# Performance work log

Measured on AMD Instinct MI355X. Metric: run time of the kernel, lower is better.

## Reference

```python
import jax, jax.numpy as jnp
import numpy as np

BIAS = 1.0
SIGMA = 0.5
EPS = 1e-5


def mrf_loss(gen, target):
    # gen, target: [B, C, H, W]
    mean_t = jnp.mean(target, axis=1, keepdims=True)
    gf = gen - mean_t
    tf = target - mean_t
    gn = gf / jnp.linalg.norm(gf, axis=1, keepdims=True)
    tn = tf / jnp.linalg.norm(tf, axis=1, keepdims=True)
    B, C, H, W = target.shape
    # 1x1 patches of target, ordered by spatial position (matches unfold h,w order)
    patches = tn.transpose(0, 2, 3, 1).reshape(B, H * W, C)  # [B, P, C]
    # per-sample conv2d with 1x1 kernels == batched GEMM
    sim = jnp.einsum('bpc,bchw->bphw', patches, gn)  # [B, P, H, W]
    cosine_dist = -(sim - 1.0) / 2.0
    relative = cosine_dist / (jnp.min(cosine_dist, axis=1, keepdims=True) + EPS)
    dist = jnp.exp((BIAS - relative) / SIGMA)
    cs = dist / jnp.sum(dist, axis=1, keepdims=True)
    k_max = jnp.max(cs.reshape(B, H * W, -1), axis=2)  # [B, P]
    div_mrf = jnp.mean(k_max, axis=1)  # [B]
    return jnp.sum(-jnp.log(div_mrf))


def setup_inputs() -> dict:
    key = jax.random.key(0)
    k1, k2, k3, k4 = jax.random.split(key, 4)
    return {
        'gen_relu3_2': jax.random.normal(k1, (4, 256, 64, 64), dtype=jnp.float32),
        'tar_relu3_2': jax.random.normal(k2, (4, 256, 64, 64), dtype=jnp.float32),
        'gen_relu4_2': jax.random.normal(k3, (4, 512, 32, 32), dtype=jnp.float32),
        'tar_relu4_2': jax.random.normal(k4, (4, 512, 32, 32), dtype=jnp.float32),
    }


def reference(gen_relu3_2, tar_relu3_2, gen_relu4_2, tar_relu4_2):
    # style layers: relu3_2 (w=1.0), relu4_2 (w=1.0); content layers: relu4_2 (w=1.0)
    m3 = mrf_loss(gen_relu3_2, tar_relu3_2)
    m4 = mrf_loss(gen_relu4_2, tar_relu4_2)
    style_loss = (1.0 * m3 + 1.0 * m4) * 1.0  # l_s = 1.0
    content_loss = (1.0 * m4) * 1.0           # l_c = 1.0
    return style_loss + content_loss
```

## Files before the change

kernel.cpp:

```cpp
#include <hip/hip_runtime.h>
#include <math.h>


#define MRF_EPS 1e-5f
#define LOG2E 1.44269504088896340736f

typedef __attribute__((ext_vector_type(8))) short bf16x8;
typedef __attribute__((ext_vector_type(4))) float f32x4;
typedef unsigned short ushort_t;
struct __align__(8) ushort4_t { ushort_t x, y, z, w; };
struct __align__(16) ushort8_t { ushort_t v[8]; };

__device__ __forceinline__ ushort_t f2bf(float x) {
    unsigned u = __float_as_uint(x);
    u += 0x7FFFu + ((u >> 16) & 1u);
    return (ushort_t)(u >> 16);
}
__device__ __forceinline__ float bf2f(ushort_t u) {
    return __uint_as_float(((unsigned)u) << 16);
}

typedef __attribute__((address_space(1))) const unsigned int gu32;
typedef __attribute__((address_space(3))) unsigned int lu32;
__device__ __forceinline__ void gload16(const ushort_t* g, ushort_t* l) {
    __builtin_amdgcn_global_load_lds((gu32*)(uintptr_t)g, (lu32*)(uintptr_t)l,
                                     16, 0, 0);
}

template <int C>
__device__ __forceinline__ void prep_body(
    const float* __restrict__ gen, const float* __restrict__ tar,
    ushort_t* __restrict__ gnT, ushort_t* __restrict__ tnT,
    int S, int b, int bx, char* __restrict__ smem) {
    constexpr int KN = C / 64;
    constexpr int KC = C / 8;
    constexpr int CP = C + 8;
    const int tid = threadIdx.x, pq = tid & 3, cs = tid >> 2;
    const int s0 = bx * 16;

    f32x4* red  = (f32x4*)smem;
    f32x4* red2 = (f32x4*)(smem + 16384);
    ushort_t* tileG = (ushort_t*)smem;
    ushort_t* tileT = tileG + 16 * CP;
    float* sm  = (float*)(smem + 33280);
    float* srt = sm + 16;
    float* srg = sm + 32;

    const float* g = gen + (size_t)b * C * S + s0 + pq * 4;
    const float* t = tar + (size_t)b * C * S + s0 + pq * 4;

    f32x4 gv[KN], tv[KN];
    f32x4 st = {0.f, 0.f, 0.f, 0.f}, st2 = st, sg = st, sg2 = st;
#pragma unroll
    for (int k = 0; k < KN; k++) {
        tv[k] = *(const f32x4*)(t + (size_t)(cs + 64 * k) * S);
        gv[k] = *(const f32x4*)(g + (size_t)(cs + 64 * k) * S);
        st += tv[k]; st2 += tv[k] * tv[k]; sg += gv[k]; sg2 += gv[k] * gv[k];
    }
    red[(0 * 4 + pq) * 64 + cs] = st;  red[(1 * 4 + pq) * 64 + cs] = st2;
    red[(2 * 4 + pq) * 64 + cs] = sg;  red[(3 * 4 + pq) * 64 + cs] = sg2;
    __syncthreads();
    if (tid < 64) {
        int s_ = tid >> 4, p_ = (tid >> 2) & 3, part = tid & 3;
        f32x4 s = red[(s_ * 4 + p_) * 64 + part * 16];
#pragma unroll
        for (int j = 1; j < 16; j++) s += red[(s_ * 4 + p_) * 64 + part * 16 + j];
        red2[(s_ * 4 + p_) * 4 + part] = s;
    }
    __syncthreads();
    if (tid < 4) {
        f32x4 sts  = red2[(0*4+tid)*4+0] + red2[(0*4+tid)*4+1] + red2[(0*4+tid)*4+2] + red2[(0*4+tid)*4+3];
        f32x4 st2s = red2[(1*4+tid)*4+0] + red2[(1*4+tid)*4+1] + red2[(1*4+tid)*4+2] + red2[(1*4+tid)*4+3];
        f32x4 sgs  = red2[(2*4+tid)*4+0] + red2[(2*4+tid)*4+1] + red2[(2*4+tid)*4+2] + red2[(2*4+tid)*4+3];
        f32x4 sg2s = red2[(3*4+tid)*4+0] + red2[(3*4+tid)*4+1] + red2[(3*4+tid)*4+2] + red2[(3*4+tid)*4+3];
        f32x4 m, vrt, vrg;
        float invC = 1.f / (float)C;
#pragma unroll
        for (int e = 0; e < 4; e++) {
            float mm = sts[e] * invC;
            m[e] = mm;
            vrt[e] = rsqrtf(st2s[e] - mm * sts[e]);
            vrg[e] = rsqrtf(sg2s[e] - 2.f * mm * sgs[e] + mm * sts[e]);
        }
        *(f32x4*)&sm[tid * 4] = m;
        *(f32x4*)&srt[tid * 4] = vrt;
        *(f32x4*)&srg[tid * 4] = vrg;
    }
    __syncthreads();
    f32x4 m4  = *(f32x4*)&sm[pq * 4];
    f32x4 rt4 = *(f32x4*)&srt[pq * 4];
    f32x4 rg4 = *(f32x4*)&srg[pq * 4];
#pragma unroll
    for (int k = 0; k < KN; k++) {
        int c = cs + 64 * k;
#pragma unroll
        for (int e = 0; e < 4; e++) {
            tileG[(pq * 4 + e) * CP + c] = f2bf((gv[k][e] - m4[e]) * rg4[e]);
            tileT[(pq * 4 + e) * CP + c] = f2bf((tv[k][e] - m4[e]) * rt4[e]);
        }
    }
    __syncthreads();
    const int lm = tid & 15;
    const int r16 = s0 >> 4;
    size_t obase = (size_t)b * (size_t)S * C;
#pragma unroll
    for (int j = 0; j < KC / 16; j++) {
        int ch = (tid >> 4) + 16 * j;
        size_t off = obase + (((size_t)r16 * KC + ch) * 16 + lm) * 8;
        *(ushort8_t*)(gnT + off) = *(const ushort8_t*)&tileG[lm * CP + ch * 8];
        *(ushort8_t*)(tnT + off) = *(const ushort8_t*)&tileT[lm * CP + ch * 8];
    }
}

__global__ __launch_bounds__(256) void prep_all(
    const float* __restrict__ gen3, const float* __restrict__ tar3,
    const float* __restrict__ gen4, const float* __restrict__ tar4,
    ushort_t* __restrict__ gnT3, ushort_t* __restrict__ tnT3,
    ushort_t* __restrict__ gnT4, ushort_t* __restrict__ tnT4) {
    __shared__ __align__(16) char smem[33536];
    int bid = blockIdx.x;
    if (bid < 256) {
        int z = bid >> 6, bx = bid & 63;
        prep_body<512>(gen4, tar4, gnT4, tnT4, 1024, z, bx, smem);
    } else {
        bid -= 256;
        int z = bid >> 8, bx = bid & 255;
        prep_body<256>(gen3, tar3, gnT3, tnT3, 4096, z, bx, smem);
    }
}

template <int K>
__device__ __forceinline__ void gemm_body(
    const ushort_t* __restrict__ A, const ushort_t* __restrict__ B,
    ushort_t* __restrict__ sim, float* __restrict__ cmPart,
    int S, int bx, int by, ushort_t* __restrict__ lds) {
    const int tid = threadIdx.x;
    const int lane = tid & 63, wave = tid >> 6;
    const int wm = (wave & 1) * 64, wn = (wave >> 1) * 64;
    const int lm = lane & 15, quad = lane >> 4;
    const int q0 = bx * 128;

    constexpr int KC = K / 8;
    constexpr int KB = K / 32;

    const ushort_t* segsrc[4];
    ushort_t* segdst[4];
#pragma unroll
    for (int i = 0; i < 4; i++) {
        int s = wave * 4 + i;
        segsrc[i] = (s < 8)
            ? A + ((size_t)(by * 8 + s) * KC) * 128 + lane * 8
            : B + ((size_t)(bx * 8 + (s - 8)) * KC) * 128 + lane * 8;
        segdst[i] = lds + s * 512;
    }

    auto stage = [&](int buf, int kb) {
#pragma unroll
        for (int i = 0; i < 4; i++)
            gload16(segsrc[i] + (size_t)kb * 512, segdst[i] + buf * 8192);
    };

    f32x4 acc[4][4];
#pragma unroll
    for (int t = 0; t < 4; t++)
#pragma unroll
        for (int u = 0; u < 4; u++) acc[t][u] = (f32x4){0.f, 0.f, 0.f, 0.f};

    stage(0, 0);
    stage(1, 1);
    asm volatile("s_waitcnt vmcnt(4)" ::: "memory");
    __builtin_amdgcn_s_barrier();
    __builtin_amdgcn_sched_barrier(0);

    const ushort_t* lA = lds + (wm >> 4) * 512 + quad * 128 + lm * 8;
    const ushort_t* lB = lds + 4096 + (wn >> 4) * 512 + quad * 128 + lm * 8;

#pragma unroll
    for (int kb = 0; kb < KB; kb++) {
        const int cur = (kb % 3) * 8192;
        if (kb + 2 < KB) stage((kb + 2) % 3, kb + 2);
        bf16x8 a[4], b[4];
#pragma unroll
        for (int t = 0; t < 4; t++) {
            a[t] = *(const bf16x8*)(lA + cur + t * 512);
            b[t] = *(const bf16x8*)(lB + cur + t * 512);
        }
        __builtin_amdgcn_s_setprio(1);
#pragma unroll
        for (int t = 0; t < 4; t++)
#pragma unroll
            for (int u = 0; u < 4; u++)
                acc[t][u] = __builtin_amdgcn_mfma_f32_16x16x32_bf16(a[t], b[u], acc[t][u], 0, 0, 0);
        __builtin_amdgcn_s_setprio(0);
        if (kb + 1 < KB) {
            if (kb + 2 < KB) asm volatile("s_waitcnt vmcnt(4)" ::: "memory");
            else             asm volatile("s_waitcnt vmcnt(0)" ::: "memory");
            __builtin_amdgcn_s_barrier();
            __builtin_amdgcn_sched_barrier(0);
        }
    }

    int nQB = S >> 7;
    size_t base = ((size_t)(by * nQB + bx)) * 16384
                + (size_t)(wave * 4096 + quad * 64 + lm * 4);
    float cmax[4] = {-INFINITY, -INFINITY, -INFINITY, -INFINITY};
#pragma unroll
    for (int t = 0; t < 4; t++)
#pragma unroll
        for (int u = 0; u < 4; u++) {
            f32x4 v = acc[t][u];
            ushort4_t o;
            o.x = f2bf(v.x); o.y = f2bf(v.y); o.z = f2bf(v.z); o.w = f2bf(v.w);
            *(ushort4_t*)(sim + base + (t * 4 + u) * 256) = o;
            float mx = fmaxf(fmaxf(bf2f(o.x), bf2f(o.y)), fmaxf(bf2f(o.z), bf2f(o.w)));
            cmax[u] = fmaxf(cmax[u], mx);
        }
    int r = by * 2 + (wave & 1);
#pragma unroll
    for (int u = 0; u < 4; u++) {
        float m = cmax[u];
        m = fmaxf(m, __shfl_xor(m, 16, 64));
        m = fmaxf(m, __shfl_xor(m, 32, 64));
        if (lane < 16) cmPart[(size_t)r * S + q0 + wn + u * 16 + lane] = m;
    }
}

__global__ __launch_bounds__(256) void gemm_all(
    const ushort_t* __restrict__ tnT3, const ushort_t* __restrict__ gnT3,
    ushort_t* __restrict__ sim3, float* __restrict__ cmPart3,
    const ushort_t* __restrict__ tnT4, const ushort_t* __restrict__ gnT4,
    ushort_t* __restrict__ sim4, float* __restrict__ cmPart4) {
    __shared__ ushort_t lds[24576];
    int bid = blockIdx.x;
    if (bid < 256) {
        int z = bid >> 6, rem = bid & 63, by = rem >> 3, bx = rem & 7;
        gemm_body<512>(tnT4 + (size_t)z * 524288, gnT4 + (size_t)z * 524288,
                       sim4 + (size_t)z * 1048576, cmPart4 + (size_t)z * 16384,
                       1024, bx, by, lds);
    } else {
        bid -= 256;
        int z = bid >> 10, rem = bid & 1023, by = rem >> 5, bx = rem & 31;
        gemm_body<256>(tnT3 + (size_t)z * 1048576, gnT3 + (size_t)z * 1048576,
                       sim3 + (size_t)z * 16777216, cmPart3 + (size_t)z * 262144,
                       4096, bx, by, lds);
    }
}

__global__ __launch_bounds__(256) void colmax_reduce_all(
    const float* __restrict__ cmPart3, float2* __restrict__ coef3, float* __restrict__ colsum3,
    const float* __restrict__ cmPart4, float2* __restrict__ coef4, float* __restrict__ colsum4,
    float* __restrict__ acc) {
    const float* cmPart; float2* coef; float* colsum; int S, R, qb, accIdx;
    int bid = blockIdx.x;
    if (bid < 16) {
        int z = bid >> 2; qb = bid & 3; S = 1024; R = 16; accIdx = 4 + z;
        cmPart = cmPart4 + (size_t)z * 16384; coef = coef4 + (size_t)z * 1024;
        colsum = colsum4 + (size_t)z * 1024;
    } else {
        bid -= 16;
        int z = bid >> 4; qb = bid & 15; S = 4096; R = 64; accIdx = z;
        cmPart = cmPart3 + (size_t)z * 262144; coef = coef3 + (size_t)z * 4096;
        colsum = colsum3 + (size_t)z * 4096;
    }
    if (qb == 0 && threadIdx.x == 0) acc[accIdx] = 0.f;
    int q = qb * 256 + threadIdx.x;
    float m = cmPart[q];
    for (int r = 1; r < R; r++) m = fmaxf(m, cmPart[(size_t)r * S + q]);
    float c1 = 1.f / ((1.f - m) * 0.5f + MRF_EPS);
    coef[q] = make_float2((2.f - c1) * LOG2E, c1 * LOG2E);
    colsum[q] = 0.f;
}

__global__ __launch_bounds__(256) void colsum_all(
    const ushort_t* __restrict__ sim3, const float2* __restrict__ coef3, float* __restrict__ colsum3,
    const ushort_t* __restrict__ sim4, const float2* __restrict__ coef4, float* __restrict__ colsum4) {
    const ushort_t* sim; const float2* coef; float* colsum; int S, bx, by;
    int bid = blockIdx.x;
    if (bid < 256) {
        int z = bid >> 6, rem = bid & 63; by = rem >> 3; bx = rem & 7; S = 1024;
        sim = sim4 + (size_t)z * 1048576; coef = coef4 + (size_t)z * 1024;
        colsum = colsum4 + (size_t)z * 1024;
    } else {
        bid -= 256;
        int z = bid >> 10, rem = bid & 1023; by = rem >> 5; bx = rem & 31; S = 4096;
        sim = sim3 + (size_t)z * 16777216; coef = coef3 + (size_t)z * 4096;
        colsum = colsum3 + (size_t)z * 4096;
    }
    int tid = threadIdx.x, lane = tid & 63;
    int u = lane >> 4, lm = lane & 15;
    int sub = (tid >> 6) & 1, cg = tid >> 7;
    int nQB = S >> 7;
    int q = bx * 128 + cg * 64 + u * 16 + lm;
    float2 cc = coef[q];
    float c0 = cc.x, c1 = cc.y;
    const ushort_t* base = sim + ((size_t)(by * nQB + bx)) * 16384
                         + (size_t)((sub | (cg << 1)) * 4096 + u * 256 + lm * 4);
    float s = 0.f;
#pragma unroll
    for (int t = 0; t < 4; t++)
#pragma unroll
        for (int quad = 0; quad < 4; quad++) {
            ushort4_t w = *(const ushort4_t*)(base + t * 1024 + quad * 64);
            s += exp2f(c0 + c1 * bf2f(w.x)) + exp2f(c0 + c1 * bf2f(w.y))
               + exp2f(c0 + c1 * bf2f(w.z)) + exp2f(c0 + c1 * bf2f(w.w));
        }
    atomicAdd(colsum + q, s);
}

__global__ __launch_bounds__(256) void rowmax_all(
    const ushort_t* __restrict__ sim3, const float2* __restrict__ coef3, const float* __restrict__ colsum3,
    const ushort_t* __restrict__ sim4, const float2* __restrict__ coef4, const float* __restrict__ colsum4,
    float* __restrict__ acc) {
    const ushort_t* sim; const float2* coef; const float* colsum;
    int S, blk; float* accSlot;
    int bid = blockIdx.x;
    if (bid < 1024) {
        int z = bid >> 8; blk = bid & 255; S = 4096; accSlot = acc + z;
        sim = sim3 + (size_t)z * 16777216; coef = coef3 + (size_t)z * 4096;
        colsum = colsum3 + (size_t)z * 4096;
    } else {
        bid -= 1024;
        int z = bid >> 6; blk = bid & 63; S = 1024; accSlot = acc + 4 + z;
        sim = sim4 + (size_t)z * 1048576; coef = coef4 + (size_t)z * 1024;
        colsum = colsum4 + (size_t)z * 1024;
    }
    int wave = threadIdx.x >> 6, lane = threadIdx.x & 63;
    int g = blk * 4 + wave;
    int by = g >> 5, rem = g & 31;
    int sub = rem >> 4, t = (rem >> 2) & 3, quad = rem & 3;
    int u = lane >> 4, lm = lane & 15;
    int nQB = S >> 7;
    f32x4 m = {-INFINITY, -INFINITY, -INFINITY, -INFINITY};
    for (int bx = 0; bx < nQB; bx++) {
#pragma unroll
        for (int cg = 0; cg < 2; cg++) {
            int q = bx * 128 + cg * 64 + u * 16 + lm;
            float2 cc = coef[q];
            float c0p = cc.x - log2f(colsum[q]);
            const ushort_t* ptr = sim + ((size_t)(by * nQB + bx)) * 16384
                                + (size_t)((sub | (cg << 1)) * 4096 + (t * 4 + u) * 256 + quad * 64 + lm * 4);
            ushort4_t w = *(const ushort4_t*)ptr;
            m[0] = fmaxf(m[0], c0p + cc.y * bf2f(w.x));
            m[1] = fmaxf(m[1], c0p + cc.y * bf2f(w.y));
            m[2] = fmaxf(m[2], c0p + cc.y * bf2f(w.z));
            m[3] = fmaxf(m[3], c0p + cc.y * bf2f(w.w));
        }
    }
#pragma unroll
    for (int off = 32; off >= 1; off >>= 1)
#pragma unroll
        for (int e = 0; e < 4; e++)
            m[e] = fmaxf(m[e], __shfl_xor(m[e], off, 64));
    __shared__ float partial[4];
    if (lane == 0)
        partial[wave] = exp2f(m[0]) + exp2f(m[1]) + exp2f(m[2]) + exp2f(m[3]);
    __syncthreads();
    if (threadIdx.x == 0)
        atomicAdd(accSlot, partial[0] + partial[1] + partial[2] + partial[3]);
}

__global__ void finalize_kernel(const float* __restrict__ acc, float* __restrict__ out) {
    float loss = 0.f;
    for (int b = 0; b < 4; b++) loss += -logf(acc[b] * (1.f / 4096.f));
    for (int b = 0; b < 4; b++) loss += -2.f * logf(acc[4 + b] * (1.f / 1024.f));
    out[0] = loss;
}

extern "C" void kernel_launch(void* const* d_in, const int* in_sizes, int n_in,
                              void* d_out, int out_size, void* d_ws, size_t ws_size,
                              hipStream_t stream) {
    const float* gen3 = (const float*)d_in[0];
    const float* tar3 = (const float*)d_in[1];
    const float* gen4 = (const float*)d_in[2];
    const float* tar4 = (const float*)d_in[3];

    char* wsb = (char*)d_ws;
    size_t off = 0;
    auto alloc = [&](size_t bytes) {
        void* p = wsb + off;
        off += (bytes + 255) & ~(size_t)255;
        return p;
    };
    ushort_t* sim3 = (ushort_t*)alloc((size_t)4 * 16777216 * 2);
    ushort_t* gnT3 = (ushort_t*)alloc((size_t)4 * 1048576 * 2);
    ushort_t* tnT3 = (ushort_t*)alloc((size_t)4 * 1048576 * 2);
    float* cmPart3 = (float*)alloc((size_t)4 * 262144 * 4);
    float2* coef3 = (float2*)alloc((size_t)4 * 4096 * 8);
    float* colsum3 = (float*)alloc((size_t)4 * 4096 * 4);
    ushort_t* sim4 = (ushort_t*)alloc((size_t)4 * 1048576 * 2);
    ushort_t* gnT4 = (ushort_t*)alloc((size_t)4 * 524288 * 2);
    ushort_t* tnT4 = (ushort_t*)alloc((size_t)4 * 524288 * 2);
    float* cmPart4 = (float*)alloc((size_t)4 * 16384 * 4);
    float2* coef4 = (float2*)alloc((size_t)4 * 1024 * 8);
    float* colsum4 = (float*)alloc((size_t)4 * 1024 * 4);
    float* acc = (float*)alloc(64 * 4);

    prep_all<<<256 + 1024, 256, 0, stream>>>(
        gen3, tar3, gen4, tar4, gnT3, tnT3, gnT4, tnT4);
    gemm_all<<<256 + 4096, 256, 0, stream>>>(
        tnT3, gnT3, sim3, cmPart3, tnT4, gnT4, sim4, cmPart4);
    colmax_reduce_all<<<16 + 64, 256, 0, stream>>>(
        cmPart3, coef3, colsum3, cmPart4, coef4, colsum4, acc);
    colsum_all<<<256 + 4096, 256, 0, stream>>>(
        sim3, coef3, colsum3, sim4, coef4, colsum4);
    rowmax_all<<<1024 + 256, 256, 0, stream>>>(
        sim3, coef3, colsum3, sim4, coef4, colsum4, acc);
    finalize_kernel<<<1, 1, 0, stream>>>(acc, (float*)d_out);
}
```

Before: 219.1 us.

## Widen sim tile layout to 16-byte stores and split rowmax across column groups

The GEMM epilogue now packs two accumulator tiles into 16-byte bf16 stores, so the sim intermediate is written and read with wider accesses. colsum and rowmax are rewritten to match: colsum reduces across lanes before its atomics, and rowmax splits the column range into groups that write partial maxima, followed by a new reduction kernel. Block indices in prep and gemm are also remapped to interleave work across XCDs. The aim is fewer memory transactions on the large sim buffer and more parallelism in rowmax, at the cost of an extra launch and a partial-max buffer.

```diff
diff --git a/kernel.cpp b/kernel.cpp
--- a/kernel.cpp
+++ b/kernel.cpp
@@ -118,7 +118,7 @@
     ushort_t* __restrict__ gnT3, ushort_t* __restrict__ tnT3,
     ushort_t* __restrict__ gnT4, ushort_t* __restrict__ tnT4) {
     __shared__ __align__(16) char smem[33536];
-    int bid = blockIdx.x;
+    int bid = (blockIdx.x & 7) * 160 + (blockIdx.x >> 3);
     if (bid < 256) {
         int z = bid >> 6, bx = bid & 63;
         prep_body<512>(gen4, tar4, gnT4, tnT4, 1024, z, bx, smem);
@@ -202,17 +202,19 @@
 
     int nQB = S >> 7;
     size_t base = ((size_t)(by * nQB + bx)) * 16384
-                + (size_t)(wave * 4096 + quad * 64 + lm * 4);
+                + (size_t)(wave * 4096 + quad * 128 + lm * 8);
     float cmax[4] = {-INFINITY, -INFINITY, -INFINITY, -INFINITY};
 #pragma unroll
-    for (int t = 0; t < 4; t++)
+    for (int t2 = 0; t2 < 2; t2++)
 #pragma unroll
         for (int u = 0; u < 4; u++) {
-            f32x4 v = acc[t][u];
-            ushort4_t o;
-            o.x = f2bf(v.x); o.y = f2bf(v.y); o.z = f2bf(v.z); o.w = f2bf(v.w);
-            *(ushort4_t*)(sim + base + (t * 4 + u) * 256) = o;
-            float mx = fmaxf(fmaxf(bf2f(o.x), bf2f(o.y)), fmaxf(bf2f(o.z), bf2f(o.w)));
+            f32x4 v0 = acc[t2 * 2][u], v1 = acc[t2 * 2 + 1][u];
+            ushort8_t o;
+            o.v[0] = f2bf(v0.x); o.v[1] = f2bf(v0.y); o.v[2] = f2bf(v0.z); o.v[3] = f2bf(v0.w);
+            o.v[4] = f2bf(v1.x); o.v[5] = f2bf(v1.y); o.v[6] = f2bf(v1.z); o.v[7] = f2bf(v1.w);
+            *(ushort8_t*)(sim + base + (t2 * 4 + u) * 512) = o;
+            float mx = fmaxf(fmaxf(fmaxf(bf2f(o.v[0]), bf2f(o.v[1])), fmaxf(bf2f(o.v[2]), bf2f(o.v[3]))),
+                             fmaxf(fmaxf(bf2f(o.v[4]), bf2f(o.v[5])), fmaxf(bf2f(o.v[6]), bf2f(o.v[7]))));
             cmax[u] = fmaxf(cmax[u], mx);
         }
     int r = by * 2 + (wave & 1);
@@ -231,7 +233,7 @@
     const ushort_t* __restrict__ tnT4, const ushort_t* __restrict__ gnT4,
     ushort_t* __restrict__ sim4, float* __restrict__ cmPart4) {
     __shared__ ushort_t lds[24576];
-    int bid = blockIdx.x;
+    int bid = (blockIdx.x & 7) * 544 + (blockIdx.x >> 3);
     if (bid < 256) {
         int z = bid >> 6, rem = bid & 63, by = rem >> 3, bx = rem & 7;
         gemm_body<512>(tnT4 + (size_t)z * 524288, gnT4 + (size_t)z * 524288,
@@ -287,76 +289,131 @@
         colsum = colsum3 + (size_t)z * 4096;
     }
     int tid = threadIdx.x, lane = tid & 63;
-    int u = lane >> 4, lm = lane & 15;
+    int quad = lane >> 4, lm = lane & 15;
     int sub = (tid >> 6) & 1, cg = tid >> 7;
+    int slot = sub | (cg << 1);
     int nQB = S >> 7;
-    int q = bx * 128 + cg * 64 + u * 16 + lm;
-    float2 cc = coef[q];
-    float c0 = cc.x, c1 = cc.y;
+    int qb = bx * 128 + cg * 64 + lm;
+    float c0[4], c1[4], su[4];
+#pragma unroll
+    for (int u = 0; u < 4; u++) {
+        float2 cc = coef[qb + u * 16];
+        c0[u] = cc.x; c1[u] = cc.y; su[u] = 0.f;
+    }
     const ushort_t* base = sim + ((size_t)(by * nQB + bx)) * 16384
-                         + (size_t)((sub | (cg << 1)) * 4096 + u * 256 + lm * 4);
-    float s = 0.f;
-#pragma unroll
-    for (int t = 0; t < 4; t++)
-#pragma unroll
-        for (int quad = 0; quad < 4; quad++) {
-            ushort4_t w = *(const ushort4_t*)(base + t * 1024 + quad * 64);
-            s += exp2f(c0 + c1 * bf2f(w.x)) + exp2f(c0 + c1 * bf2f(w.y))
-               + exp2f(c0 + c1 * bf2f(w.z)) + exp2f(c0 + c1 * bf2f(w.w));
-        }
-    atomicAdd(colsum + q, s);
+                         + (size_t)(slot * 4096 + quad * 128 + lm * 8);
+#pragma unroll
+    for (int t2 = 0; t2 < 2; t2++)
+#pragma unroll
+        for (int u = 0; u < 4; u++) {
+            ushort8_t e = *(const ushort8_t*)(base + (t2 * 4 + u) * 512);
+            float s = 0.f;
+#pragma unroll
+            for (int j = 0; j < 8; j++) s += exp2f(c0[u] + c1[u] * bf2f(e.v[j]));
+            su[u] += s;
+        }
+#pragma unroll
+    for (int u = 0; u < 4; u++) {
+        su[u] += __shfl_xor(su[u], 16, 64);
+        su[u] += __shfl_xor(su[u], 32, 64);
+        if (lane < 16) atomicAdd(colsum + qb + u * 16, su[u]);
+    }
+}
+
+template <int NQB, int NBX>
+__device__ __forceinline__ void rowmax_body(
+    const ushort_t* __restrict__ sim, const float2* __restrict__ coef,
+    const float* __restrict__ colsum, float* __restrict__ rmPart,
+    int by, int g) {
+    int tid = threadIdx.x, lane = tid & 63, wave = tid >> 6;
+    int ph = wave & 1, t2 = wave >> 1;
+    int quad = lane >> 4, lm = lane & 15;
+    float m[8];
+#pragma unroll
+    for (int j = 0; j < 8; j++) m[j] = -INFINITY;
+    for (int bxi = 0; bxi < NBX; bxi++) {
+        int bx = g * NBX + bxi;
+        float c0p[8], c1v[8];
+#pragma unroll
+        for (int cg = 0; cg < 2; cg++)
+#pragma unroll
+            for (int u = 0; u < 4; u++) {
+                int q = bx * 128 + cg * 64 + u * 16 + lm;
+                float2 cc = coef[q];
+                c0p[cg * 4 + u] = cc.x - log2f(colsum[q]);
+                c1v[cg * 4 + u] = cc.y;
+            }
+        const ushort_t* bb = sim + ((size_t)(by * NQB + bx)) * 16384
+                           + (size_t)((t2 * 4) * 512 + quad * 128 + lm * 8);
+#pragma unroll
+        for (int cg = 0; cg < 2; cg++) {
+            int slot = ph + 2 * cg;
+#pragma unroll
+            for (int u = 0; u < 4; u++) {
+                ushort8_t e = *(const ushort8_t*)(bb + slot * 4096 + u * 512);
+                float a = c0p[cg * 4 + u], c = c1v[cg * 4 + u];
+#pragma unroll
+                for (int j = 0; j < 8; j++) m[j] = fmaxf(m[j], a + c * bf2f(e.v[j]));
+            }
+        }
+    }
+#pragma unroll
+    for (int off = 1; off <= 8; off <<= 1)
+#pragma unroll
+        for (int j = 0; j < 8; j++) m[j] = fmaxf(m[j], __shfl_xor(m[j], off, 64));
+    if (lm == 0) {
+        int pbase = by * 128 + ph * 64 + t2 * 32 + quad * 4;
+#pragma unroll
+        for (int j = 0; j < 8; j++)
+            rmPart[pbase + (j >> 2) * 16 + (j & 3)] = m[j];
+    }
 }
 
 __global__ __launch_bounds__(256) void rowmax_all(
     const ushort_t* __restrict__ sim3, const float2* __restrict__ coef3, const float* __restrict__ colsum3,
+    float* __restrict__ rmPart3,
     const ushort_t* __restrict__ sim4, const float2* __restrict__ coef4, const float* __restrict__ colsum4,
-    float* __restrict__ acc) {
-    const ushort_t* sim; const float2* coef; const float* colsum;
-    int S, blk; float* accSlot;
+    float* __restrict__ rmPart4) {
     int bid = blockIdx.x;
     if (bid < 1024) {
-        int z = bid >> 8; blk = bid & 255; S = 4096; accSlot = acc + z;
-        sim = sim3 + (size_t)z * 16777216; coef = coef3 + (size_t)z * 4096;
-        colsum = colsum3 + (size_t)z * 4096;
+        int z = bid >> 8, rem = bid & 255, by = rem >> 3, g = rem & 7;
+        rowmax_body<32, 4>(sim3 + (size_t)z * 16777216, coef3 + (size_t)z * 4096,
+                           colsum3 + (size_t)z * 4096,
+                           rmPart3 + ((size_t)(z * 8 + g)) * 4096, by, g);
     } else {
         bid -= 1024;
-        int z = bid >> 6; blk = bid & 63; S = 1024; accSlot = acc + 4 + z;
-        sim = sim4 + (size_t)z * 1048576; coef = coef4 + (size_t)z * 1024;
-        colsum = colsum4 + (size_t)z * 1024;
-    }
-    int wave = threadIdx.x >> 6, lane = threadIdx.x & 63;
-    int g = blk * 4 + wave;
-    int by = g >> 5, rem = g & 31;
-    int sub = rem >> 4, t = (rem >> 2) & 3, quad = rem & 3;
-    int u = lane >> 4, lm = lane & 15;
-    int nQB = S >> 7;
-    f32x4 m = {-INFINITY, -INFINITY, -INFINITY, -INFINITY};
-    for (int bx = 0; bx < nQB; bx++) {
-#pragma unroll
-        for (int cg = 0; cg < 2; cg++) {
-            int q = bx * 128 + cg * 64 + u * 16 + lm;
-            float2 cc = coef[q];
-            float c0p = cc.x - log2f(colsum[q]);
-            const ushort_t* ptr = sim + ((size_t)(by * nQB + bx)) * 16384
-                                + (size_t)((sub | (cg << 1)) * 4096 + (t * 4 + u) * 256 + quad * 64 + lm * 4);
-            ushort4_t w = *(const ushort4_t*)ptr;
-            m[0] = fmaxf(m[0], c0p + cc.y * bf2f(w.x));
-            m[1] = fmaxf(m[1], c0p + cc.y * bf2f(w.y));
-            m[2] = fmaxf(m[2], c0p + cc.y * bf2f(w.z));
-            m[3] = fmaxf(m[3], c0p + cc.y * bf2f(w.w));
-        }
-    }
-#pragma unroll
-    for (int off = 32; off >= 1; off >>= 1)
-#pragma unroll
-        for (int e = 0; e < 4; e++)
-            m[e] = fmaxf(m[e], __shfl_xor(m[e], off, 64));
-    __shared__ float partial[4];
-    if (lane == 0)
-        partial[wave] = exp2f(m[0]) + exp2f(m[1]) + exp2f(m[2]) + exp2f(m[3]);
+        int z = bid >> 5, rem = bid & 31, by = rem >> 2, g = rem & 3;
+        rowmax_body<8, 2>(sim4 + (size_t)z * 1048576, coef4 + (size_t)z * 1024,
+                          colsum4 + (size_t)z * 1024,
+                          rmPart4 + ((size_t)(z * 4 + g)) * 1024, by, g);
+    }
+}
+
+__global__ __launch_bounds__(256) void rmreduce_all(
+    const float* __restrict__ rmPart3, const float* __restrict__ rmPart4,
+    float* __restrict__ acc) {
+    const float* rm; int G, stride, p; float* slot;
+    int bid = blockIdx.x;
+    if (bid < 64) {
+        int z = bid >> 4, blk = bid & 15; G = 8; stride = 4096;
+        rm = rmPart3 + (size_t)z * 8 * 4096;
+        p = blk * 256 + threadIdx.x; slot = acc + z;
+    } else {
+        bid -= 64;
+        int z = bid >> 2, blk = bid & 3; G = 4; stride = 1024;
+        rm = rmPart4 + (size_t)z * 4 * 1024;
+        p = blk * 256 + threadIdx.x; slot = acc + 4 + z;
+    }
+    float m = rm[p];
+    for (int g = 1; g < G; g++) m = fmaxf(m, rm[(size_t)g * stride + p]);
+    float k = exp2f(m);
+#pragma unroll
+    for (int off = 32; off >= 1; off >>= 1) k += __shfl_xor(k, off, 64);
+    __shared__ float part[4];
+    if ((threadIdx.x & 63) == 0) part[threadIdx.x >> 6] = k;
     __syncthreads();
     if (threadIdx.x == 0)
-        atomicAdd(accSlot, partial[0] + partial[1] + partial[2] + partial[3]);
+        atomicAdd(slot, part[0] + part[1] + part[2] + part[3]);
 }
 
 __global__ void finalize_kernel(const float* __restrict__ acc, float* __restrict__ out) {
@@ -387,12 +444,14 @@
     float* cmPart3 = (float*)alloc((size_t)4 * 262144 * 4);
     float2* coef3 = (float2*)alloc((size_t)4 * 4096 * 8);
     float* colsum3 = (float*)alloc((size_t)4 * 4096 * 4);
+    float* rmPart3 = (float*)alloc((size_t)4 * 8 * 4096 * 4);
     ushort_t* sim4 = (ushort_t*)alloc((size_t)4 * 1048576 * 2);
     ushort_t* gnT4 = (ushort_t*)alloc((size_t)4 * 524288 * 2);
     ushort_t* tnT4 = (ushort_t*)alloc((size_t)4 * 524288 * 2);
     float* cmPart4 = (float*)alloc((size_t)4 * 16384 * 4);
     float2* coef4 = (float2*)alloc((size_t)4 * 1024 * 8);
     float* colsum4 = (float*)alloc((size_t)4 * 1024 * 4);
+    float* rmPart4 = (float*)alloc((size_t)4 * 4 * 1024 * 4);
     float* acc = (float*)alloc(64 * 4);
 
     prep_all<<<256 + 1024, 256, 0, stream>>>(
@@ -403,7 +462,8 @@
         cmPart3, coef3, colsum3, cmPart4, coef4, colsum4, acc);
     colsum_all<<<256 + 4096, 256, 0, stream>>>(
         sim3, coef3, colsum3, sim4, coef4, colsum4);
-    rowmax_all<<<1024 + 256, 256, 0, stream>>>(
-        sim3, coef3, colsum3, sim4, coef4, colsum4, acc);
+    rowmax_all<<<1024 + 128, 256, 0, stream>>>(
+        sim3, coef3, colsum3, rmPart3, sim4, coef4, colsum4, rmPart4);
+    rmreduce_all<<<64 + 16, 256, 0, stream>>>(rmPart3, rmPart4, acc);
     finalize_kernel<<<1, 1, 0, stream>>>(acc, (float*)d_out);
 }
```

Measured after the change: 220.8 us. Within noise of the previous version (+0.8%).
